# Optimization experiments

Measured on AMD Instinct MI355X. Metric: run time of the kernel, lower is better.

The kernel has to match this reference:

```python
import jax, jax.numpy as jnp
import numpy as np

B, S, D = 32, 512, 768
DSYM, DROLE = 32, 32
H = DSYM * DROLE  # LSTM hidden = out_dim = dSymbols*dRoles
NSYM, NROLE = 50, 35
TEMP = 1.0


def setup_inputs() -> dict:
    key = jax.random.key(0)
    ks = jax.random.split(key, 12)
    n = lambda k, shp, s=0.02: jax.random.normal(k, shp, dtype=jnp.float32) * s
    return {
        "x": jax.random.normal(ks[0], (B, S, D), dtype=jnp.float32),
        "WihF": n(ks[1], (4 * H, D)), "WhhF": n(ks[2], (4 * H, H)),
        "bihF": jnp.zeros((4 * H,), jnp.float32), "bhhF": jnp.zeros((4 * H,), jnp.float32),
        "WihR": n(ks[3], (4 * H, D)), "WhhR": n(ks[4], (4 * H, H)),
        "bihR": jnp.zeros((4 * H,), jnp.float32), "bhhR": jnp.zeros((4 * H,), jnp.float32),
        "WaF_w": n(ks[5], (NSYM, H)), "WaF_b": jnp.zeros((NSYM,), jnp.float32),
        "WaR_w": n(ks[6], (NROLE, H)), "WaR_b": jnp.zeros((NROLE,), jnp.float32),
        "F_w": n(ks[7], (DSYM, NSYM)), "R_w": n(ks[8], (DROLE, NROLE)),
        "scale_F": jnp.float32(1.0), "scale_R": jnp.float32(1.0),
    }


def _lstm_cell(x_t, h, c, Wih, Whh, bih, bhh):
    # PyTorch LSTM gate order: i, f, g, o
    g = x_t @ Wih.T + bih + h @ Whh.T + bhh  # [B, 4H]
    i, f, gg, o = jnp.split(g, 4, axis=-1)
    c = jax.nn.sigmoid(f) * c + jax.nn.sigmoid(i) * jnp.tanh(gg)
    h = jax.nn.sigmoid(o) * jnp.tanh(c)
    return h, c


def reference(x, WihF, WhhF, bihF, bhhF, WihR, WhhR, bihR, bhhR,
              WaF_w, WaF_b, WaR_w, WaR_b, F_w, R_w, scale_F, scale_R):
    batch = x.shape[0]

    def step(carry, x_t):
        T, cF, cR = carry  # hidden h of BOTH cells is overwritten by TPR binding T
        hF, cF = _lstm_cell(x_t, T, cF, WihF, WhhF, bihF, bhhF)
        hR, cR = _lstm_cell(x_t, T, cR, WihR, WhhR, bihR, bhhR)
        aF = jax.nn.softmax((hF @ WaF_w.T + WaF_b) / TEMP, axis=-1)  # [B, NSYM]
        aR = jax.nn.softmax((hR @ WaR_w.T + WaR_b) / TEMP, axis=-1)  # [B, NROLE]
        itemF = scale_F * (aF @ F_w.T)  # [B, DSYM]  (ScaleLinear, no bias)
        itemR = scale_R * (aR @ R_w.T)  # [B, DROLE]
        Tn = jnp.einsum('bs,br->bsr', itemF, itemR).reshape(batch, H)
        return (Tn, cF, cR), (Tn, aF, aR)

    z = jnp.zeros((batch, H), x.dtype)
    _, (outs, aFs, aRs) = jax.lax.scan(step, (z, z, z), jnp.swapaxes(x, 0, 1))
    # back to batch-first: out [B,S,H], aFs [B,S,NSYM], aRs [B,S,NROLE]
    return (jnp.swapaxes(outs, 0, 1), jnp.swapaxes(aFs, 0, 1), jnp.swapaxes(aRs, 0, 1))
```

## Files before the change

### kernel.cpp

```cpp
#include <hip/hip_runtime.h>
#include <stdint.h>
#include <stddef.h>

#define B_   32
#define S_   512
#define D_   768
#define H_   1024
#define NF_  50
#define NR_  35
#define NRP_ 36
#define NWG  256
#define WGS  256

#define RTAG_OFF  32768
#define ITB_OFF   40960
#define PF_OFF    65536
#define XBF_OFF   1703936
#define PF_F_SZ   102400
#define PF_STEP   176128

typedef __attribute__((ext_vector_type(8))) short sh8;
typedef __attribute__((ext_vector_type(4))) float f4;
typedef __attribute__((ext_vector_type(2))) float f2v;
typedef __attribute__((ext_vector_type(4))) unsigned int u4x;
typedef unsigned long long u64;

__device__ __forceinline__ unsigned short f2bf(float f) {
  unsigned int u = __float_as_uint(f);
  u += 0x7fffu + ((u >> 16) & 1u);
  return (unsigned short)(u >> 16);
}

__device__ __forceinline__ unsigned cvtpk_bf16(float lo, float hi) {
  unsigned r;
  asm("v_cvt_pk_bf16_f32 %0, %1, %2" : "=v"(r) : "v"(lo), "v"(hi));
  return r;
}

__device__ __forceinline__ sh8 cvt8(const float* __restrict__ p) {
  f4 av = *(const f4*)p;
  f4 bv = *(const f4*)(p + 4);
  union { sh8 s; unsigned short us[8]; } r;
  r.us[0] = f2bf(av[0]); r.us[1] = f2bf(av[1]); r.us[2] = f2bf(av[2]); r.us[3] = f2bf(av[3]);
  r.us[4] = f2bf(bv[0]); r.us[5] = f2bf(bv[1]); r.us[6] = f2bf(bv[2]); r.us[7] = f2bf(bv[3]);
  return r.s;
}

__device__ __forceinline__ float sigm(float x) { return 1.f / (1.f + __expf(-x)); }

__device__ __forceinline__ float tanhfast(float x) {
  const float e = __expf(2.f * x);
  return 1.f - 2.f / (e + 1.f);
}

__device__ __forceinline__ u64 pack2(float a, float b) {
  return (u64)__float_as_uint(a) | ((u64)__float_as_uint(b) << 32);
}

template<int NA, int NPAIR>
__device__ __forceinline__ void pf_store(int tid, int wIdx, int b0,
                                         const float* __restrict__ h_lds,
                                         const float* __restrict__ Wa_l,
                                         u64* __restrict__ d64) {
  const int tot = 16 * NPAIR;
  for (int i = tid; i < tot; i += WGS) {
    const int bl = i / NPAIR, k = i - bl * NPAIR;
    const int n0 = 2 * k, n1 = 2 * k + 1;
    float v0 = 0.f, v1 = 0.f;
    #pragma unroll
    for (int jj = 0; jj < 16; ++jj) v0 += h_lds[bl * 16 + jj] * Wa_l[n0 * 17 + jj];
    if (n1 < NA) {
      #pragma unroll
      for (int jj = 0; jj < 16; ++jj) v1 += h_lds[bl * 16 + jj] * Wa_l[n1 * 17 + jj];
    }
    __hip_atomic_store(&d64[(size_t)((b0 + bl) * 64 + wIdx) * NPAIR + k], pack2(v0, v1),
                       __ATOMIC_RELAXED, __HIP_MEMORY_SCOPE_AGENT);
  }
}

template<int NAR, int NAPR>
__device__ __forceinline__ void reduce_tail(
    int tid, int wave, int lane,
    const u64* __restrict__ src64, float* __restrict__ stage,
    float (* __restrict__ red4)[64], float* __restrict__ arow,
    const float* __restrict__ bA, const float* __restrict__ WL, float sc,
    float* __restrict__ itRow, unsigned int* __restrict__ rtagLine, unsigned stag,
    float* __restrict__ outRow)
{
  u64* st64 = (u64*)stage;
  constexpr int n64 = (64 * NAPR) >> 1;
  for (int i = tid; i < n64; i += WGS)
    st64[i] = __hip_atomic_load(&src64[i], __ATOMIC_RELAXED, __HIP_MEMORY_SCOPE_AGENT);
  __syncthreads();
  {
    const int n = (lane < NAR) ? lane : 0;
    float v = 0.f;
    #pragma unroll
    for (int w2 = 0; w2 < 16; ++w2) v += stage[(wave * 16 + w2) * NAPR + n];
    red4[wave][lane] = v;
  }
  __syncthreads();
  if (wave == 0) {
    const int n = (lane < NAR) ? lane : 0;
    const float v = red4[0][lane] + red4[1][lane] + red4[2][lane] + red4[3][lane];
    float e = (lane < NAR) ? __expf(v + bA[n]) : 0.f;
    float ssum = e;
    #pragma unroll
    for (int off = 1; off < 64; off <<= 1) ssum += __shfl_xor(ssum, off, 64);
    const float a = e / ssum;
    if (lane < NAR) arow[lane] = a;
    {
      constexpr int KH = (NAR + 1) >> 1;
      const int dr = lane & 31;
      float it = 0.f;
      if (lane < 32) {
        #pragma unroll
        for (int k = 0; k < KH; ++k) it += arow[k] * WL[dr * NAR + k];
      } else {
        #pragma unroll
        for (int k = KH; k < NAR; ++k) it += arow[k] * WL[dr * NAR + k];
      }
      it += __shfl_xor(it, 32, 64);
      if (lane < 32)
        __hip_atomic_store(&itRow[lane], it * sc, __ATOMIC_RELAXED, __HIP_MEMORY_SCOPE_AGENT);
    }
    if (lane == 0) {
      __asm__ __volatile__("s_waitcnt vmcnt(0)" ::: "memory");
      __hip_atomic_store(rtagLine, stag, __ATOMIC_RELAXED, __HIP_MEMORY_SCOPE_AGENT);
    }
    if (lane < NAR) outRow[lane] = a;
  }
}

__global__ void init_ws(unsigned int* __restrict__ flags) {
  const int t = blockIdx.x * blockDim.x + threadIdx.x;
  const int stride = gridDim.x * blockDim.x;
  for (int i = t; i < 10240; i += stride)
    __hip_atomic_store(&flags[i], 0u, __ATOMIC_RELAXED, __HIP_MEMORY_SCOPE_AGENT);
}

__global__ void xcvt(const float* __restrict__ x, unsigned int* __restrict__ xb2, int ndw) {
  const int stride = gridDim.x * blockDim.x;
  for (int o = blockIdx.x * blockDim.x + threadIdx.x; o < ndw; o += stride) {
    const int e2  = o & 3;
    const int l   = (o >> 2) & 63;
    const int tb  = o >> 8;
    const int t   = tb % 24;
    const int bts = tb / 24;
    const int bt  = bts & 1;
    const int s   = bts >> 1;
    const int b   = bt * 16 + (l & 15);
    const int k   = t * 32 + (l >> 4) * 8 + e2 * 2;
    const f2v v = ((const f2v*)x)[(((size_t)b * S_ + s) * D_ + k) >> 1];
    xb2[o] = (unsigned int)f2bf(v[0]) | ((unsigned int)f2bf(v[1]) << 16);
  }
}

__global__ __launch_bounds__(WGS, 1) void tpr_persist(
    const float* __restrict__ x, const unsigned short* __restrict__ xbf, int xmode,
    const float* __restrict__ WihF, const float* __restrict__ WhhF,
    const float* __restrict__ bihF, const float* __restrict__ bhhF,
    const float* __restrict__ WihR, const float* __restrict__ WhhR,
    const float* __restrict__ bihR, const float* __restrict__ bhhR,
    const float* __restrict__ WaFw, const float* __restrict__ WaFb,
    const float* __restrict__ WaRw, const float* __restrict__ WaRb,
    const float* __restrict__ Fw, const float* __restrict__ Rw,
    const float* __restrict__ scFp, const float* __restrict__ scRp,
    float* __restrict__ out0, unsigned char* __restrict__ ws)
{
  __shared__ __align__(16) float part[4][16 * 69];
  __shared__ float h_lds[16 * 16];
  __shared__ __align__(16) float itF_l[16 * 36];
  __shared__ __align__(16) float itR_l[16 * 36];
  __shared__ float Fw_l[32 * NF_];
  __shared__ float Rw_l[32 * NR_];
  __shared__ float Wa_l[NF_ * 17];
  __shared__ float red4[4][64];
  __shared__ float arow[64];
  __shared__ float bias_l[64];
  __shared__ float bF_l[NF_];
  __shared__ float bR_l[NR_];

  const int wg    = blockIdx.x;
  const int tid   = threadIdx.x;
  const int wave  = tid >> 6;
  const int lane  = tid & 63;
  const int n16   = lane & 15;
  const int quad  = lane >> 4;
  const int group = wg >> 6;
  const bool isF  = wg < 128;
  const int hb    = group & 1;
  const int b0    = hb * 16;
  const int wIdx  = wg & 63;
  const int j0    = wIdx * 16;
  const int gbase = group << 6;
  const float* Wih = isF ? WihF : WihR;
  const float* Whh = isF ? WhhF : WhhR;
  const float* bih = isF ? bihF : bihR;
  const float* bhh = isF ? bhhF : bhhR;
  const float* Wa  = isF ? WaFw : WaRw;
  const int NA  = isF ? NF_ : NR_;

  unsigned int* wtag = (unsigned int*)ws;
  unsigned int* rtag = (unsigned int*)(ws + RTAG_OFF);
  float* itBuf = (float*)(ws + ITB_OFF);
  float* pf    = (float*)(ws + PF_OFF);

  sh8 whhf[4][8];
  sh8 wihf[4][6];
  #pragma unroll
  for (int g = 0; g < 4; ++g) {
    const int row = g * 1024 + j0 + n16;
    #pragma unroll
    for (int ks = 0; ks < 8; ++ks)
      whhf[g][ks] = cvt8(Whh + (size_t)row * H_ + wave * 256 + ks * 32 + quad * 8);
    #pragma unroll
    for (int ks = 0; ks < 6; ++ks)
      wihf[g][ks] = cvt8(Wih + (size_t)row * D_ + wave * 192 + ks * 32 + quad * 8);
  }

  if (tid < 64) {
    const int row = (tid >> 4) * 1024 + j0 + (tid & 15);
    bias_l[tid] = bih[row] + bhh[row];
  }
  for (int i = tid; i < NA * 16; i += WGS)
    Wa_l[(i >> 4) * 17 + (i & 15)] = Wa[(size_t)(i >> 4) * H_ + j0 + (i & 15)];
  for (int i = tid; i < 32 * NF_; i += WGS) Fw_l[i] = Fw[i];
  for (int i = tid; i < 32 * NR_; i += WGS) Rw_l[i] = Rw[i];
  if (tid < NF_) bF_l[tid] = WaFb[tid];
  if (tid < NR_) bR_l[tid] = WaRb[tid];
  const float sF = scFp[0];
  const float sR = scRp[0];
  float cc = 0.f;

  f4 xacc[4];
  const f4 fz = {0.f, 0.f, 0.f, 0.f};

  auto xpart = [&](int sx) {
    #pragma unroll
    for (int g = 0; g < 4; ++g) xacc[g] = fz;
    #pragma unroll
    for (int ks = 0; ks < 6; ++ks) {
      sh8 xa;
      if (xmode == 0) {
        const size_t toff = ((size_t)((sx * 2 + hb) * 24 + wave * 6 + ks) << 9)
                            + (size_t)lane * 8;
        union { u4x u; sh8 s; } t;
        t.u = *(const u4x*)(xbf + toff);
        xa = t.s;
      } else {
        const size_t off = ((size_t)(b0 + n16) * S_ + sx) * D_ + wave * 192 + ks * 32 + quad * 8;
        xa = cvt8(x + off);
      }
      #pragma unroll
      for (int g = 0; g < 4; ++g)
        xacc[g] = __builtin_amdgcn_mfma_f32_16x16x32_bf16(xa, wihf[g][ks], xacc[g], 0, 0, 0);
    }
  };

  xpart(0);
  __syncthreads();

  float* out1 = out0 + (size_t)B_ * S_ * H_;
  float* out2 = out1 + (size_t)B_ * S_ * NF_;

  const bool isRed = (wIdx < 16);
  const int  redB  = b0 + wIdx;
  const bool redF  = isF;
  const int  redJ  = (redF ? 0 : 32) + redB;

  for (int s = 0; s < S_; ++s) {
    const int buf = s & 1;
    const unsigned int stag = (unsigned int)(s + 1);

    f4 acc[4];
    #pragma unroll
    for (int g = 0; g < 4; ++g) acc[g] = xacc[g];
    if (s > 0) {
      const f4 fA0 = *(const f4*)&itF_l[n16 * 36 + (wave << 3)];
      const f4 fA1 = *(const f4*)&itF_l[n16 * 36 + (wave << 3) + 4];
      const f4 rA0 = *(const f4*)&itR_l[n16 * 36 + (quad << 3)];
      const f4 rA1 = *(const f4*)&itR_l[n16 * 36 + (quad << 3) + 4];
      #pragma unroll
      for (int ks = 0; ks < 8; ++ks) {
        const float fs = (ks < 4) ? fA0[ks & 3] : fA1[ks & 3];
        union { sh8 s8; u4x u; } t;
        t.u[0] = cvtpk_bf16(fs * rA0[0], fs * rA0[1]);
        t.u[1] = cvtpk_bf16(fs * rA0[2], fs * rA0[3]);
        t.u[2] = cvtpk_bf16(fs * rA1[0], fs * rA1[1]);
        t.u[3] = cvtpk_bf16(fs * rA1[2], fs * rA1[3]);
        #pragma unroll
        for (int g = 0; g < 4; ++g)
          acc[g] = __builtin_amdgcn_mfma_f32_16x16x32_bf16(t.s8, whhf[g][ks], acc[g], 0, 0, 0);
      }
    }
    #pragma unroll
    for (int g = 0; g < 4; ++g)
      #pragma unroll
      for (int r = 0; r < 4; ++r)
        part[wave][(quad * 4 + r) * 69 + g * 16 + n16] = acc[g][r];
    __syncthreads();

    {
      const int bl = tid >> 4;
      const int jj = tid & 15;
      float G[4];
      #pragma unroll
      for (int g = 0; g < 4; ++g) {
        const int n = g * 16 + jj;
        G[g] = bias_l[n] + part[0][bl * 69 + n] + part[1][bl * 69 + n]
                         + part[2][bl * 69 + n] + part[3][bl * 69 + n];
      }
      const float ig = sigm(G[0]);
      const float fg = sigm(G[1]);
      const float gg = tanhfast(G[2]);
      const float og = sigm(G[3]);
      cc = fg * cc + ig * gg;
      h_lds[bl * 16 + jj] = og * tanhfast(cc);
    }
    __syncthreads();

    if (isF)
      pf_store<NF_, (NF_ >> 1)>(tid, wIdx, b0, h_lds, Wa_l,
          (u64*)(pf + (size_t)buf * PF_STEP));
    else
      pf_store<NR_, (NRP_ >> 1)>(tid, wIdx, b0, h_lds, Wa_l,
          (u64*)(pf + (size_t)buf * PF_STEP + PF_F_SZ));
    __syncthreads();
    if (tid == 0)
      __hip_atomic_store(&wtag[wg * 32], stag, __ATOMIC_RELAXED, __HIP_MEMORY_SCOPE_AGENT);

    if (isRed) {
      if (wave == 0) {
        for (;;) {
          const unsigned int v = __hip_atomic_load(&wtag[(gbase + lane) * 32],
                                                   __ATOMIC_RELAXED, __HIP_MEMORY_SCOPE_AGENT);
          if (__ballot(v >= stag) == ~0ull) break;
          __builtin_amdgcn_s_sleep(1);
        }
      }
      __syncthreads();
      if (redF)
        reduce_tail<NF_, NF_>(tid, wave, lane,
            (const u64*)(pf + (size_t)buf * PF_STEP + (size_t)redB * 64 * NF_),
            &part[0][0], red4, arow, bF_l, Fw_l, sF,
            &itBuf[((size_t)buf * 64 + redJ) * 32], &rtag[redJ * 32], stag,
            &out1[((size_t)redB * S_ + s) * NF_]);
      else
        reduce_tail<NR_, NRP_>(tid, wave, lane,
            (const u64*)(pf + (size_t)buf * PF_STEP + PF_F_SZ + (size_t)redB * 64 * NRP_),
            &part[0][0], red4, arow, bR_l, Rw_l, sR,
            &itBuf[((size_t)buf * 64 + redJ) * 32], &rtag[redJ * 32], stag,
            &out2[((size_t)redB * S_ + s) * NR_]);
    }

    if (s + 1 < S_) xpart(s + 1);

    if (wave == 0) {
      const int sub = lane & 31;
      const int row = (sub < 16) ? (b0 + sub) : (32 + b0 + (sub - 16));
      for (;;) {
        const unsigned int v = __hip_atomic_load(&rtag[row * 32],
                                                 __ATOMIC_RELAXED, __HIP_MEMORY_SCOPE_AGENT);
        if (__ballot(v >= stag) == ~0ull) break;
        __builtin_amdgcn_s_sleep(1);
      }
    }
    __syncthreads();

    {
      const u64* s64 = (const u64*)itBuf;
      for (int i = tid; i < 512; i += WGS) {
        const int lr = i >> 4;
        const int c64 = i & 15;
        const int grow = (lr < 16) ? (b0 + lr) : (32 + b0 + (lr - 16));
        const u64 p = __hip_atomic_load(&s64[((size_t)buf * 64 + grow) * 16 + c64],
                                        __ATOMIC_RELAXED, __HIP_MEMORY_SCOPE_AGENT);
        const float lo = __uint_as_float((unsigned int)p);
        const float hi = __uint_as_float((unsigned int)(p >> 32));
        const int c4 = 2 * c64;
        if (lr < 16) { itF_l[lr * 36 + c4] = lo; itF_l[lr * 36 + c4 + 1] = hi; }
        else         { itR_l[(lr - 16) * 36 + c4] = lo; itR_l[(lr - 16) * 36 + c4 + 1] = hi; }
      }
    }
    __syncthreads();

    if (isF && wIdx >= 32 && wIdx < 48) {
      const int bl = wIdx - 32;
      const int ds = tid >> 3, dr0 = (tid & 7) * 4;
      f4 v;
      #pragma unroll
      for (int q = 0; q < 4; ++q) v[q] = itF_l[bl * 36 + ds] * itR_l[bl * 36 + dr0 + q];
      *(f4*)&out0[((size_t)(b0 + bl) * S_ + s) * H_ + tid * 4] = v;
    }
  }
}

extern "C" void kernel_launch(void* const* d_in, const int* in_sizes, int n_in,
                              void* d_out, int out_size, void* d_ws, size_t ws_size,
                              hipStream_t stream) {
  (void)in_sizes; (void)n_in; (void)out_size;
  const float* x    = (const float*)d_in[0];
  const float* WihF = (const float*)d_in[1];
  const float* WhhF = (const float*)d_in[2];
  const float* bihF = (const float*)d_in[3];
  const float* bhhF = (const float*)d_in[4];
  const float* WihR = (const float*)d_in[5];
  const float* WhhR = (const float*)d_in[6];
  const float* bihR = (const float*)d_in[7];
  const float* bihR2= (const float*)d_in[8];
  const float* WaFw = (const float*)d_in[9];
  const float* WaFb = (const float*)d_in[10];
  const float* WaRw = (const float*)d_in[11];
  const float* WaRb = (const float*)d_in[12];
  const float* Fw   = (const float*)d_in[13];
  const float* Rw   = (const float*)d_in[14];
  const float* scF  = (const float*)d_in[15];
  const float* scR  = (const float*)d_in[16];

  unsigned char* ws = (unsigned char*)d_ws;
  unsigned short* xbf = (unsigned short*)(ws + XBF_OFF);
  const size_t need = (size_t)XBF_OFF + (size_t)B_ * S_ * D_ * 2;
  const int xmode = (ws_size >= need) ? 0 : 1;

  init_ws<<<8, 256, 0, stream>>>((unsigned int*)ws);
  if (xmode == 0)
    xcvt<<<2048, 256, 0, stream>>>(x, (unsigned int*)xbf, (B_ * S_ * D_) / 2);
  tpr_persist<<<NWG, WGS, 0, stream>>>(x, xbf, xmode,
      WihF, WhhF, bihF, bhhF, WihR, WhhR, bihR, bihR2,
      WaFw, WaFb, WaRw, WaRb, Fw, Rw, scF, scR,
      (float*)d_out, ws);
}
```

Before: 4.564 ms.

## Pack item values with step tags to replace separate ready-flag handshake

Each item value written by the reducing workgroups is now stored as a 64-bit word holding the float and the step tag, so consumers poll the data words directly instead of first spinning on a separate rtag flag and then loading the data. This removes the writer-side s_waitcnt before the flag store and one global round trip plus a barrier on the consumer side of every timestep. In exchange every consumer thread polls its own words, which raises memory traffic while spinning and doubles the size of the item buffer.

Result: faster. 4.333 ms, median of 2 (-5.0%).

```diff
diff --git a/kernel.cpp b/kernel.cpp
--- a/kernel.cpp
+++ b/kernel.cpp
@@ -12,8 +12,7 @@
 #define NWG  256
 #define WGS  256
 
-#define RTAG_OFF  32768
-#define ITB_OFF   40960
+#define ITB_OFF   32768
 #define PF_OFF    65536
 #define XBF_OFF   1703936
 #define PF_F_SZ   102400
@@ -56,6 +55,12 @@
 __device__ __forceinline__ u64 pack2(float a, float b) {
   return (u64)__float_as_uint(a) | ((u64)__float_as_uint(b) << 32);
 }
+
+__device__ __forceinline__ u64 tagv(float v, unsigned t) {
+  return (u64)__float_as_uint(v) | ((u64)t << 32);
+}
+__device__ __forceinline__ float    valof(u64 p) { return __uint_as_float((unsigned)p); }
+__device__ __forceinline__ unsigned tagof(u64 p) { return (unsigned)(p >> 32); }
 
 template<int NA, int NPAIR>
 __device__ __forceinline__ void pf_store(int tid, int wIdx, int b0,
@@ -84,7 +89,7 @@
     const u64* __restrict__ src64, float* __restrict__ stage,
     float (* __restrict__ red4)[64], float* __restrict__ arow,
     const float* __restrict__ bA, const float* __restrict__ WL, float sc,
-    float* __restrict__ itRow, unsigned int* __restrict__ rtagLine, unsigned stag,
+    u64* __restrict__ itRowT, unsigned stag,
     float* __restrict__ outRow)
 {
   u64* st64 = (u64*)stage;
@@ -122,11 +127,8 @@
       }
       it += __shfl_xor(it, 32, 64);
       if (lane < 32)
-        __hip_atomic_store(&itRow[lane], it * sc, __ATOMIC_RELAXED, __HIP_MEMORY_SCOPE_AGENT);
-    }
-    if (lane == 0) {
-      __asm__ __volatile__("s_waitcnt vmcnt(0)" ::: "memory");
-      __hip_atomic_store(rtagLine, stag, __ATOMIC_RELAXED, __HIP_MEMORY_SCOPE_AGENT);
+        __hip_atomic_store(&itRowT[lane], tagv(it * sc, stag),
+                           __ATOMIC_RELAXED, __HIP_MEMORY_SCOPE_AGENT);
     }
     if (lane < NAR) outRow[lane] = a;
   }
@@ -135,7 +137,7 @@
 __global__ void init_ws(unsigned int* __restrict__ flags) {
   const int t = blockIdx.x * blockDim.x + threadIdx.x;
   const int stride = gridDim.x * blockDim.x;
-  for (int i = t; i < 10240; i += stride)
+  for (int i = t; i < 16384; i += stride)
     __hip_atomic_store(&flags[i], 0u, __ATOMIC_RELAXED, __HIP_MEMORY_SCOPE_AGENT);
 }
 
@@ -202,8 +204,7 @@
   const int NA  = isF ? NF_ : NR_;
 
   unsigned int* wtag = (unsigned int*)ws;
-  unsigned int* rtag = (unsigned int*)(ws + RTAG_OFF);
-  float* itBuf = (float*)(ws + ITB_OFF);
+  u64* itb = (u64*)(ws + ITB_OFF);
   float* pf    = (float*)(ws + PF_OFF);
 
   sh8 whhf[4][8];
@@ -344,43 +345,50 @@
         reduce_tail<NF_, NF_>(tid, wave, lane,
             (const u64*)(pf + (size_t)buf * PF_STEP + (size_t)redB * 64 * NF_),
             &part[0][0], red4, arow, bF_l, Fw_l, sF,
-            &itBuf[((size_t)buf * 64 + redJ) * 32], &rtag[redJ * 32], stag,
+            &itb[((size_t)buf * 64 + redJ) * 32], stag,
             &out1[((size_t)redB * S_ + s) * NF_]);
       else
         reduce_tail<NR_, NRP_>(tid, wave, lane,
             (const u64*)(pf + (size_t)buf * PF_STEP + PF_F_SZ + (size_t)redB * 64 * NRP_),
             &part[0][0], red4, arow, bR_l, Rw_l, sR,
-            &itBuf[((size_t)buf * 64 + redJ) * 32], &rtag[redJ * 32], stag,
+            &itb[((size_t)buf * 64 + redJ) * 32], stag,
             &out2[((size_t)redB * S_ + s) * NR_]);
     }
 
     if (s + 1 < S_) xpart(s + 1);
 
-    if (wave == 0) {
-      const int sub = lane & 31;
-      const int row = (sub < 16) ? (b0 + sub) : (32 + b0 + (sub - 16));
-      for (;;) {
-        const unsigned int v = __hip_atomic_load(&rtag[row * 32],
-                                                 __ATOMIC_RELAXED, __HIP_MEMORY_SCOPE_AGENT);
-        if (__ballot(v >= stag) == ~0ull) break;
+    {
+      const u64* src = itb + (size_t)buf * 64 * 32;
+      float vals[4];
+      unsigned sm = 0;
+      #pragma unroll
+      for (int k2 = 0; k2 < 4; ++k2) {
+        const int i = tid + k2 * WGS;
+        const int lr = i >> 5, col = i & 31;
+        const int grow = (lr < 16) ? (b0 + lr) : (32 + b0 + (lr - 16));
+        const u64 p = __hip_atomic_load(&src[(size_t)grow * 32 + col],
+                                        __ATOMIC_RELAXED, __HIP_MEMORY_SCOPE_AGENT);
+        vals[k2] = valof(p);
+        sm |= (tagof(p) != stag) ? (1u << k2) : 0u;
+      }
+      while (sm) {
         __builtin_amdgcn_s_sleep(1);
-      }
-    }
-    __syncthreads();
-
-    {
-      const u64* s64 = (const u64*)itBuf;
-      for (int i = tid; i < 512; i += WGS) {
-        const int lr = i >> 4;
-        const int c64 = i & 15;
-        const int grow = (lr < 16) ? (b0 + lr) : (32 + b0 + (lr - 16));
-        const u64 p = __hip_atomic_load(&s64[((size_t)buf * 64 + grow) * 16 + c64],
-                                        __ATOMIC_RELAXED, __HIP_MEMORY_SCOPE_AGENT);
-        const float lo = __uint_as_float((unsigned int)p);
-        const float hi = __uint_as_float((unsigned int)(p >> 32));
-        const int c4 = 2 * c64;
-        if (lr < 16) { itF_l[lr * 36 + c4] = lo; itF_l[lr * 36 + c4 + 1] = hi; }
-        else         { itR_l[(lr - 16) * 36 + c4] = lo; itR_l[(lr - 16) * 36 + c4 + 1] = hi; }
+        #pragma unroll
+        for (int k2 = 0; k2 < 4; ++k2) if (sm & (1u << k2)) {
+          const int i = tid + k2 * WGS;
+          const int lr = i >> 5, col = i & 31;
+          const int grow = (lr < 16) ? (b0 + lr) : (32 + b0 + (lr - 16));
+          const u64 p = __hip_atomic_load(&src[(size_t)grow * 32 + col],
+                                          __ATOMIC_RELAXED, __HIP_MEMORY_SCOPE_AGENT);
+          if (tagof(p) == stag) { vals[k2] = valof(p); sm &= ~(1u << k2); }
+        }
+      }
+      #pragma unroll
+      for (int k2 = 0; k2 < 4; ++k2) {
+        const int i = tid + k2 * WGS;
+        const int lr = i >> 5, col = i & 31;
+        if (lr < 16) itF_l[lr * 36 + col] = vals[k2];
+        else         itR_l[(lr - 16) * 36 + col] = vals[k2];
       }
     }
     __syncthreads();
```
